# Kernel optimization log

Measured on AMD Instinct MI355X. Metric: run time of the kernel, lower is better.

The kernel has to match this reference:

```python
import jax, jax.numpy as jnp
import numpy as np

C = 64        # channel_n
HID = 128     # hidden_size
HEADS = 4
HD = 16       # head_dim = embed_dim // heads, embed_dim overwritten to channel_n
INNER = HEADS * HD  # 64
MLP = 64
H = W = 64    # img_size
B = 8
STEPS = 6
IN_CH = 1     # input_channels
SCALE = HD ** -0.5


def conv3x3_reflect(x, w, b):
    # x: [B,C,H,W], w: [O,I,3,3] -- reflect padding like nn.Conv2d(padding_mode='reflect')
    xp = jnp.pad(x, ((0, 0), (0, 0), (1, 1), (1, 1)), mode='reflect')
    y = jax.lax.conv_general_dilated(xp, w, (1, 1), 'VALID',
                                     dimension_numbers=('NCHW', 'OIHW', 'NCHW'))
    return y + b[None, :, None, None]


def layernorm(x, w, b, axes):
    mu = jnp.mean(x, axis=axes, keepdims=True)
    var = jnp.var(x, axis=axes, keepdims=True)
    return (x - mu) * jax.lax.rsqrt(var + 1e-5) * w + b


def localize(t, h, w):
    # t: [B,heads,n,d] -> [B,heads,n,9,d]; zero-padded 3x3 neighbourhoods
    # (equivalent to grouped conv with 9 unit-impulse filters, padding='same')
    b, nh, n, d = t.shape
    g = t.reshape(b, nh, h, w, d)
    gp = jnp.pad(g, ((0, 0), (0, 0), (1, 1), (1, 1), (0, 0)))
    nb = jnp.stack([gp[:, :, i:i + h, j:j + w, :]
                    for i in range(3) for j in range(3)], axis=4)
    return nb.reshape(b, nh, n, 9, d)


def attn_block(t, ln_w, ln_b, qkv_w, out_w, out_b):
    y = layernorm(t, ln_w, ln_b, -1)
    qkv = y @ qkv_w.T                              # [B,n,3*inner]
    q, k, v = jnp.split(qkv, 3, axis=-1)
    to_heads = lambda z: z.reshape(z.shape[0], z.shape[1], HEADS, HD).transpose(0, 2, 1, 3)
    q, k, v = to_heads(q), to_heads(k), to_heads(v)   # [B,h,n,d]
    kl = localize(k, H, W)                          # [B,h,n,9,d]
    vl = localize(v, H, W)
    dots = jnp.einsum('bhnd,bhnkd->bhnk', q, kl) * SCALE
    a = jax.nn.softmax(dots, axis=-1)               # [B,h,n,9]
    o = jnp.einsum('bhnk,bhnkd->bhnd', a, vl)
    o = o.transpose(0, 2, 1, 3).reshape(t.shape[0], t.shape[1], INNER)
    return o @ out_w.T + out_b


def ff_block(t, ln_w, ln_b, w1, b1, w2, b2):
    y = layernorm(t, ln_w, ln_b, -1)
    y = jax.nn.gelu(y @ w1.T + b1, approximate=False)
    return y @ w2.T + b2


def setup_inputs() -> dict:
    key = jax.random.key(0)
    ks = jax.random.split(key, 20)
    s = 0.02
    inp = {
        'x': jax.random.normal(ks[0], (B, H, W, C), jnp.float32),
        'masks': jax.random.bernoulli(ks[1], 0.5, (STEPS, B, H, W, 1)),
        'p0_w': jax.random.normal(ks[2], (C, C, 3, 3)) * s,
        'p0_b': jnp.zeros((C,)),
        'p1_w': jax.random.normal(ks[3], (C, C, 3, 3)) * s,
        'p1_b': jnp.zeros((C,)),
        'fc0_w': jax.random.normal(ks[4], (HID, 3 * C)) * s,
        'fc0_b': jnp.zeros((HID,)),
        'fc1_w': jax.random.normal(ks[5], (C, HID)) * s,  # zero-init in torch; random here for a non-trivial test
        'norm0_w': jnp.ones((H, W, HID)),
        'norm0_b': jnp.zeros((H, W, HID)),
        'ln1_w': jnp.ones((C,)),
        'ln1_b': jnp.zeros((C,)),
        'qkv_w': jax.random.normal(ks[6], (3 * INNER, C)) * s,
        'out_w': jax.random.normal(ks[7], (C, INNER)) * s,
        'out_b': jnp.zeros((C,)),
        'ln2_w': jnp.ones((C,)),
        'ln2_b': jnp.zeros((C,)),
        'ff1_w': jax.random.normal(ks[8], (MLP, C)) * s,
        'ff1_b': jnp.zeros((MLP,)),
        'ff2_w': jax.random.normal(ks[9], (C, MLP)) * s,
        'ff2_b': jnp.zeros((C,)),
        'steps': STEPS,
    }
    return inp


def reference(x, masks, p0_w, p0_b, p1_w, p1_b, fc0_w, fc0_b, fc1_w,
              norm0_w, norm0_b, ln1_w, ln1_b, qkv_w, out_w, out_b,
              ln2_w, ln2_b, ff1_w, ff1_b, ff2_w, ff2_b, steps):
    def step(xc, mask):
        # ---- NCA perception + update (BackboneNCA.perceive + fc0/relu/norm/fc1) ----
        xt = xc.transpose(0, 3, 1, 2)                      # [B,C,H,W]
        y1 = conv3x3_reflect(xt, p0_w, p0_b)
        y2 = conv3x3_reflect(xt, p1_w, p1_b)
        p = jnp.concatenate([xt, y1, y2], 1).transpose(0, 2, 3, 1)  # [B,H,W,3C]
        hd = jax.nn.relu(p @ fc0_w.T + fc0_b)              # [B,H,W,HID]
        hd = layernorm(hd, norm0_w, norm0_b, (-3, -2, -1))  # norm0 over [H,W,HID]
        dx = hd @ fc1_w.T                                   # [B,H,W,C]
        dx = dx * mask.astype(xc.dtype)                     # stochastic fire
        xn = xc + dx
        # ---- ViT block with localized (3x3 windowed) attention ----
        t = xn.reshape(B, H * W, C)
        t = t + attn_block(t, ln1_w, ln1_b, qkv_w, out_w, out_b)
        t = t + ff_block(t, ln2_w, ln2_b, ff1_w, ff1_b, ff2_w, ff2_b)
        xn = t.reshape(B, H, W, C)
        # keep input channels unchanged
        xn = jnp.concatenate([xc[..., :IN_CH], xn[..., IN_CH:]], axis=-1)
        return xn, None

    out, _ = jax.lax.scan(step, x, masks)
    return out
```

## Files before the change

kernel.cpp:

```cpp
#include <hip/hip_runtime.h>
#include <hip/hip_bf16.h>

typedef __hip_bfloat16 bf16;
typedef __attribute__((ext_vector_type(8))) short bf16x8;
typedef __attribute__((ext_vector_type(4))) float f32x4;

#define NSTEP 6

static __device__ __forceinline__ float b2f(bf16 v) { return __bfloat162float(v); }

static __device__ __forceinline__ float ldp(const void* p, int i, int md) {
    return md ? ((const float*)p)[i] : b2f(((const bf16*)p)[i]);
}
static __device__ __forceinline__ float finz(float v) {
    return (v == v && v * 0.0f == 0.0f) ? v : 0.0f;
}
static __device__ __forceinline__ unsigned short f2bfu(float v) {
    bf16 h = __float2bfloat16(v);
    return *(unsigned short*)&h;
}

static __device__ __forceinline__ void ld_bf8(const bf16* p, float* f) {
    union { uint4 u; unsigned short s[8]; } r;
    r.u = *(const uint4*)p;
#pragma unroll
    for (int j = 0; j < 8; ++j) f[j] = __uint_as_float(((unsigned)r.s[j]) << 16);
}
static __device__ __forceinline__ void ldp8(const void* p, int i, int md, float* f) {
    if (md) {
        const float* fp = (const float*)p + i;
        float4 a = *(const float4*)fp, b = *(const float4*)(fp + 4);
        f[0]=a.x; f[1]=a.y; f[2]=a.z; f[3]=a.w; f[4]=b.x; f[5]=b.y; f[6]=b.z; f[7]=b.w;
    } else {
        ld_bf8((const bf16*)p + i, f);
    }
}
static __device__ __forceinline__ uint4 pk_bf8(const float* f) {
    union { uint4 u; unsigned short s[8]; } r;
#pragma unroll
    for (int j = 0; j < 8; ++j) r.s[j] = f2bfu(f[j]);
    return r.u;
}


__global__ void k_detect(const uint4* __restrict__ m4,
                         const uint4* __restrict__ x4,
                         int* __restrict__ flags, float* __restrict__ accv) {
    __shared__ int s3f, sup, slo, sf32;
    int t = threadIdx.x;
    if (t == 0) { s3f = 0; sup = 0; slo = 0; sf32 = 0; }
    if (t < 96) accv[t] = 0.f;
    __syncthreads();
    int l3f = 0, lup = 0, llo = 0, lf = 0;
    for (int i = t; i < 3072; i += 256) {
        uint4 v = m4[i];
        const unsigned* d = (const unsigned*)&v;
#pragma unroll
        for (int j = 0; j < 4; ++j) {
            unsigned w = d[j];
            unsigned x3f = w ^ 0x3F3F3F3Fu;
            if ((x3f - 0x01010101u) & ~x3f & 0x80808080u) l3f = 1;
            if (w & 0xFFFFFF00u) lup = 1;
            if (w & 0x0000FFFFu) llo = 1;
        }
    }
    for (int i = t; i < 4096; i += 256) {
        uint4 v = x4[i];
        const unsigned* d = (const unsigned*)&v;
#pragma unroll
        for (int j = 0; j < 4; ++j) {
            unsigned bb = (d[j] >> 8) & 0x7Fu;
            if (bb > 0x48u) lf = 1;
        }
    }
    if (l3f) atomicOr(&s3f, 1);
    if (lup) atomicOr(&sup, 1);
    if (llo) atomicOr(&slo, 1);
    if (lf)  atomicOr(&sf32, 1);
    __syncthreads();
    if (t == 0) {
        int mode;
        if (!s3f && !sup) mode = 0;
        else if (!s3f)    mode = 1;
        else if (slo)     mode = 2;
        else              mode = 3;
        flags[0] = mode;
        flags[1] = sf32;
    }
}

__global__ void k_cast(const void* __restrict__ in, float* __restrict__ out,
                       const int* __restrict__ mflags, int n8) {
    int md = mflags[1];
    int i = blockIdx.x * 256 + threadIdx.x;
    if (i < n8) {
        float f[8];
        ldp8(in, i * 8, md, f);
#pragma unroll
        for (int j = 0; j < 8; ++j) f[j] = finz(f[j]);
        *(float4*)&out[i * 8]     = make_float4(f[0], f[1], f[2], f[3]);
        *(float4*)&out[i * 8 + 4] = make_float4(f[4], f[5], f[6], f[7]);
    }
}

__global__ void k_transpose(const void* __restrict__ in, float* __restrict__ out,
                            const int* __restrict__ mflags, int R, int K) {
    int md = mflags[1];
    int i = blockIdx.x * 256 + threadIdx.x;
    if (i < R * K) {
        int k = i / R, r = i % R;
        out[i] = ldp(in, r * K + k, md);
    }
}

__global__ void k_pack_bf16(const void* __restrict__ in, short* __restrict__ out,
                            const int* __restrict__ mflags, int n) {
    int md = mflags[1];
    int i = blockIdx.x * 256 + threadIdx.x;
    if (i < n) out[i] = (short)f2bfu(ldp(in, i, md));
}

__global__ void k_pack_bt1(const void* __restrict__ p0, const void* __restrict__ p1,
                           short* __restrict__ out, const int* __restrict__ mflags) {
    int md = mflags[1];
    int i = blockIdx.x * 256 + threadIdx.x;
    if (i < 128 * 576) {
        int o = i / 576, k = i % 576;
        int kk = k >> 6, ii = k & 63;
        float v = (o < 64) ? ldp(p0, o * 576 + ii * 9 + kk, md)
                           : ldp(p1, (o - 64) * 576 + ii * 9 + kk, md);
        out[i] = (short)f2bfu(v);
    }
}


__global__ __launch_bounds__(512) void k_perceive(
    const float* __restrict__ xin, const short* __restrict__ bt1,
    const short* __restrict__ fc0s, const void* __restrict__ p0b,
    const void* __restrict__ p1b, const void* __restrict__ fc0b,
    const int* __restrict__ mflags, bf16* __restrict__ hd,
    float* __restrict__ accv, int step)
{
    __shared__ __align__(16) short xpad_s[3 * 66 * 72];
    __shared__ __align__(16) short P_s[64 * 200];
    __shared__ float red[32];
    int md = mflags[1];
    int bh = blockIdx.x;
    int b = bh >> 6, h = bh & 63;
    int t = threadIdx.x;

    for (int e = t; e < 1536; e += 512) {
        int c8 = e & 7, w = (e >> 3) & 63, r = e >> 9;
        int hr = h - 1 + r; hr = hr < 0 ? -hr : (hr > 63 ? 126 - hr : hr);
        const float* src = xin + ((((b << 6) + hr) << 6) | w) * 64 + c8 * 8;
        float f[8];
        float4 v0 = *(const float4*)src, v1 = *(const float4*)(src + 4);
        f[0]=v0.x; f[1]=v0.y; f[2]=v0.z; f[3]=v0.w; f[4]=v1.x; f[5]=v1.y; f[6]=v1.z; f[7]=v1.w;
        uint4 pv = pk_bf8(f);
        *(uint4*)&xpad_s[((r * 66) + w + 1) * 72 + c8 * 8] = pv;
        if (r == 1) *(uint4*)&P_s[w * 200 + c8 * 8] = pv;
    }
    if (t < 48) {
        int c8 = t & 7, side = (t >> 3) & 1, r = t >> 4;
        int hr = h - 1 + r; hr = hr < 0 ? -hr : (hr > 63 ? 126 - hr : hr);
        int wsrc = side ? 62 : 1, wp = side ? 65 : 0;
        const float* src = xin + ((((b << 6) + hr) << 6) | wsrc) * 64 + c8 * 8;
        float f[8];
        float4 v0 = *(const float4*)src, v1 = *(const float4*)(src + 4);
        f[0]=v0.x; f[1]=v0.y; f[2]=v0.z; f[3]=v0.w; f[4]=v1.x; f[5]=v1.y; f[6]=v1.z; f[7]=v1.w;
        *(uint4*)&xpad_s[((r * 66) + wp) * 72 + c8 * 8] = pk_bf8(f);
    }
    __syncthreads();

    int og  = __builtin_amdgcn_readfirstlane(t >> 6);
    int l   = t & 63, nl = l & 15, q = l >> 4;
    int mt0 = (og & 1) * 2;
    int nt0 = (og >> 1) * 2;
    int o0  = nt0 * 16 + nl, o1 = o0 + 16;

    f32x4 acc[2][2];
#pragma unroll
    for (int i = 0; i < 2; ++i)
#pragma unroll
        for (int j = 0; j < 2; ++j) acc[i][j] = (f32x4){0.f, 0.f, 0.f, 0.f};

    for (int kt = 0; kt < 18; ++kt) {
        int kk = kt >> 1, c0 = (kt & 1) << 5;
        int r = kk / 3, cxi = kk - r * 3;
        bf16x8 b0 = *(const bf16x8*)(bt1 + o0 * 576 + kt * 32 + q * 8);
        bf16x8 b1 = *(const bf16x8*)(bt1 + o1 * 576 + kt * 32 + q * 8);
        bf16x8 a0 = *(const bf16x8*)&xpad_s[((r * 66) + mt0 * 16 + nl + cxi) * 72 + c0 + q * 8];
        bf16x8 a1 = *(const bf16x8*)&xpad_s[((r * 66) + mt0 * 16 + 16 + nl + cxi) * 72 + c0 + q * 8];
        acc[0][0] = __builtin_amdgcn_mfma_f32_16x16x32_bf16(a0, b0, acc[0][0], 0, 0, 0);
        acc[0][1] = __builtin_amdgcn_mfma_f32_16x16x32_bf16(a0, b1, acc[0][1], 0, 0, 0);
        acc[1][0] = __builtin_amdgcn_mfma_f32_16x16x32_bf16(a1, b0, acc[1][0], 0, 0, 0);
        acc[1][1] = __builtin_amdgcn_mfma_f32_16x16x32_bf16(a1, b1, acc[1][1], 0, 0, 0);
    }
    {
        float bias0 = (o0 < 64) ? ldp(p0b, o0, md) : ldp(p1b, o0 - 64, md);
        float bias1 = (o1 < 64) ? ldp(p0b, o1, md) : ldp(p1b, o1 - 64, md);
#pragma unroll
        for (int i = 0; i < 2; ++i)
#pragma unroll
            for (int j = 0; j < 2; ++j) {
                int oo = j ? o1 : o0;
                float bb = j ? bias1 : bias0;
#pragma unroll
                for (int r2 = 0; r2 < 4; ++r2) {
                    int m = (mt0 + i) * 16 + q * 4 + r2;
                    P_s[m * 200 + 64 + oo] = (short)f2bfu(acc[i][j][r2] + bb);
                }
            }
    }
    __syncthreads();

#pragma unroll
    for (int i = 0; i < 2; ++i)
#pragma unroll
        for (int j = 0; j < 2; ++j) acc[i][j] = (f32x4){0.f, 0.f, 0.f, 0.f};
    for (int kt = 0; kt < 6; ++kt) {
        bf16x8 b0 = *(const bf16x8*)(fc0s + o0 * 192 + kt * 32 + q * 8);
        bf16x8 b1 = *(const bf16x8*)(fc0s + o1 * 192 + kt * 32 + q * 8);
        bf16x8 a0 = *(const bf16x8*)&P_s[(mt0 * 16 + nl) * 200 + kt * 32 + q * 8];
        bf16x8 a1 = *(const bf16x8*)&P_s[(mt0 * 16 + 16 + nl) * 200 + kt * 32 + q * 8];
        acc[0][0] = __builtin_amdgcn_mfma_f32_16x16x32_bf16(a0, b0, acc[0][0], 0, 0, 0);
        acc[0][1] = __builtin_amdgcn_mfma_f32_16x16x32_bf16(a0, b1, acc[0][1], 0, 0, 0);
        acc[1][0] = __builtin_amdgcn_mfma_f32_16x16x32_bf16(a1, b0, acc[1][0], 0, 0, 0);
        acc[1][1] = __builtin_amdgcn_mfma_f32_16x16x32_bf16(a1, b1, acc[1][1], 0, 0, 0);
    }
    float lsum = 0.f, lsq = 0.f;
    {
        float fb0 = ldp(fc0b, o0, md), fb1 = ldp(fc0b, o1, md);
#pragma unroll
        for (int i = 0; i < 2; ++i)
#pragma unroll
            for (int j = 0; j < 2; ++j) {
                int oo = j ? o1 : o0;
                float bb = j ? fb1 : fb0;
#pragma unroll
                for (int r2 = 0; r2 < 4; ++r2) {
                    int m = (mt0 + i) * 16 + q * 4 + r2;
                    float v = fmaxf(acc[i][j][r2] + bb, 0.f);
                    unsigned short hu = f2bfu(v);
                    hd[((bh << 6) + m) * 128 + oo] = *(bf16*)&hu;
                    float vr = __uint_as_float(((unsigned)hu) << 16);
                    lsum += vr; lsq += vr * vr;
                }
            }
    }
#pragma unroll
    for (int off = 32; off > 0; off >>= 1) {
        lsum += __shfl_down(lsum, off, 64);
        lsq  += __shfl_down(lsq,  off, 64);
    }
    if (l == 0) { red[og] = lsum; red[16 + og] = lsq; }
    __syncthreads();
    if (t == 0) {
        float a = 0.f, s2 = 0.f;
#pragma unroll
        for (int w = 0; w < 8; ++w) { a += red[w]; s2 += red[16 + w]; }
        atomicAdd(&accv[step * 16 + b * 2],     a);
        atomicAdd(&accv[step * 16 + b * 2 + 1], s2);
    }
}

__global__ __launch_bounds__(512) void k_update_qkv(
    float* __restrict__ xio, const bf16* __restrict__ hd,
    const float* __restrict__ fc1t, const void* __restrict__ n0w,
    const void* __restrict__ n0b, const void* __restrict__ mraw,
    const int* __restrict__ mflags, const float* __restrict__ accv,
    float* __restrict__ c0buf, const float* __restrict__ qkvt,
    const void* __restrict__ ln1w, const void* __restrict__ ln1b,
    bf16* __restrict__ qkv, int step)
{
    __shared__ float hdn[64 * 129];
    __shared__ float ys[64 * 65];
    int md = mflags[1];
    int bh = blockIdx.x;
    int b = bh >> 6, h = bh & 63;
    int t = threadIdx.x;
    const float invN = 1.f / 524288.f;
    float mean = accv[step * 16 + b * 2] * invN;
    float var  = accv[step * 16 + b * 2 + 1] * invN - mean * mean;
    float rstd = rsqrtf(fmaxf(var, 0.f) + 1e-5f);

    const bf16* hrow = hd + ((b * 64 + h) * 64) * 128;
    for (int e = t; e < 1024; e += 512) {
        int pos = e >> 4, j8 = (e & 15) * 8;
        float hv[8], wv[8], bv[8];
        ld_bf8(hrow + pos * 128 + j8, hv);
        int ni = (h * 64 + pos) * 128 + j8;
        ldp8(n0w, ni, md, wv);
        ldp8(n0b, ni, md, bv);
#pragma unroll
        for (int j = 0; j < 8; ++j)
            hdn[pos * 129 + j8 + j] = (hv[j] - mean) * rstd * wv[j] + bv[j];
    }
    __syncthreads();

    int cg  = __builtin_amdgcn_readfirstlane(t >> 6);
    int pos = t & 63;
    float acc[8];
#pragma unroll
    for (int ci = 0; ci < 8; ++ci) acc[ci] = 0.f;
    for (int j = 0; j < 128; ++j) {
        float hv = hdn[pos * 129 + j];
        const float* fw = fc1t + j * 64 + cg * 8;
#pragma unroll
        for (int ci = 0; ci < 8; ++ci) acc[ci] = fmaf(fw[ci], hv, acc[ci]);
    }
    int mmode = mflags[0];
    int midx = ((step * 8 + b) * 64 + h) * 64 + pos;
    int m;
    if (mmode == 0)      m = ((const int*)mraw)[midx] != 0;
    else if (mmode == 1) m = ((const unsigned char*)mraw)[midx] != 0;
    else if (mmode == 2) m = ((const unsigned short*)mraw)[midx] != 0;
    else                 m = ((const float*)mraw)[midx] != 0.0f;

    int idx = ((b * 64 + h) * 64 + pos) * 64 + cg * 8;
    float4 x0 = *(const float4*)&xio[idx];
    float4 x1 = *(const float4*)&xio[idx + 4];
    float xv[8] = {x0.x, x0.y, x0.z, x0.w, x1.x, x1.y, x1.z, x1.w};
    if (cg == 0) c0buf[(b * 64 + h) * 64 + pos] = xv[0];
    float xn[8];
#pragma unroll
    for (int ci = 0; ci < 8; ++ci) {
        xn[ci] = finz(m ? (xv[ci] + acc[ci]) : xv[ci]);
        ys[pos * 65 + cg * 8 + ci] = xn[ci];
    }
    *(float4*)&xio[idx]     = make_float4(xn[0], xn[1], xn[2], xn[3]);
    *(float4*)&xio[idx + 4] = make_float4(xn[4], xn[5], xn[6], xn[7]);
    __syncthreads();

    {
        int tok = t >> 3, j8 = (t & 7) * 8;
        float v[8];
        float ls = 0.f, lq = 0.f;
#pragma unroll
        for (int ci = 0; ci < 8; ++ci) {
            v[ci] = ys[tok * 65 + j8 + ci];
            ls += v[ci]; lq += v[ci] * v[ci];
        }
#pragma unroll
        for (int off = 1; off < 8; off <<= 1) {
            ls += __shfl_xor(ls, off, 64);
            lq += __shfl_xor(lq, off, 64);
        }
        float mu = ls * (1.f / 64.f);
        float vr = lq * (1.f / 64.f) - mu * mu;
        float rs = rsqrtf(fmaxf(vr, 0.f) + 1e-5f);
        float wv[8], bv[8];
        ldp8(ln1w, j8, md, wv);
        ldp8(ln1b, j8, md, bv);
#pragma unroll
        for (int ci = 0; ci < 8; ++ci)
            ys[tok * 65 + j8 + ci] = (v[ci] - mu) * rs * wv[ci] + bv[ci];
    }
    __syncthreads();

    float a2[24];
#pragma unroll
    for (int oi = 0; oi < 24; ++oi) a2[oi] = 0.f;
    for (int c = 0; c < 64; ++c) {
        float yv = ys[pos * 65 + c];
        const float* qw = qkvt + c * 192 + cg * 24;
#pragma unroll
        for (int oi = 0; oi < 24; ++oi) a2[oi] = fmaf(qw[oi], yv, a2[oi]);
    }
    union { uint4 u[3]; unsigned short s[24]; } pq;
#pragma unroll
    for (int oi = 0; oi < 24; ++oi) pq.s[oi] = f2bfu(a2[oi]);
    uint4* qrow = (uint4*)(qkv + (((b * 64 + h) * 64) + pos) * 192 + cg * 24);
    qrow[0] = pq.u[0]; qrow[1] = pq.u[1]; qrow[2] = pq.u[2];
}

__global__ __launch_bounds__(512) void k_attn_ff(
    const bf16* __restrict__ qkv, float* __restrict__ xio,
    const float* __restrict__ c0buf, const short* __restrict__ outs,
    const short* __restrict__ ff1s, const short* __restrict__ ff2s,
    const void* __restrict__ outb, const void* __restrict__ ln2w,
    const void* __restrict__ ln2b, const void* __restrict__ ff1b,
    const void* __restrict__ ff2b, const int* __restrict__ mflags,
    void* __restrict__ dout, int write_out)
{
    __shared__ __align__(16) char smraw[50944];
    float* kv = (float*)smraw;
    short* Ao = (short*)smraw;
    float* ts = (float*)(smraw + 9216);
    short* ys = (short*)(smraw + 25856);
    short* hs = (short*)(smraw + 35072);

    int md = mflags[1];
    int bh = blockIdx.x;
    int b = bh >> 6, h = bh & 63;
    int t = threadIdx.x;

    if (t < 192) {
        int c = t & 63, r = t >> 6;
        kv[c * 199 + r * 66]      = 0.f;
        kv[c * 199 + r * 66 + 65] = 0.f;
    }
    for (int e = t; e < 1536; e += 512) {
        int c8 = (e & 7) * 8, w = (e >> 3) & 63, r = e >> 9;
        int hr = h - 1 + r;
        float f[8];
        if (hr >= 0 && hr <= 63) {
            ld_bf8(qkv + ((b * 64 + hr) * 64 + w) * 192 + 64 + c8, f);
        } else {
#pragma unroll
            for (int j = 0; j < 8; ++j) f[j] = 0.f;
        }
#pragma unroll
        for (int j = 0; j < 8; ++j) kv[(c8 + j) * 199 + r * 66 + w + 1] = f[j];
    }
    __syncthreads();

    int head = __builtin_amdgcn_readfirstlane((t >> 6) & 3);
    int pos  = t & 63;
    float q[16];
    {
        const bf16* qr = qkv + (((b * 64 + h) * 64) + pos) * 192 + head * 16;
        ld_bf8(qr, q); ld_bf8(qr + 8, q + 8);
    }

    float a[9];
#pragma unroll
    for (int r = 0; r < 3; ++r)
#pragma unroll
        for (int cxi = 0; cxi < 3; ++cxi) {
            float dot = 0.f;
#pragma unroll
            for (int d = 0; d < 16; ++d)
                dot = fmaf(q[d], kv[(head * 16 + d) * 199 + r * 66 + pos + cxi], dot);
            a[r * 3 + cxi] = dot * 0.25f;
        }
    float mx = a[0];
#pragma unroll
    for (int k = 1; k < 9; ++k) mx = fmaxf(mx, a[k]);
    float ssum = 0.f;
#pragma unroll
    for (int k = 0; k < 9; ++k) { a[k] = __expf(a[k] - mx); ssum += a[k]; }
    float inv = 1.f / ssum;
#pragma unroll
    for (int k = 0; k < 9; ++k) a[k] *= inv;
    __syncthreads();

    for (int e = t; e < 1536; e += 512) {
        int c8 = (e & 7) * 8, w = (e >> 3) & 63, r = e >> 9;
        int hr = h - 1 + r;
        float f[8];
        if (hr >= 0 && hr <= 63) {
            ld_bf8(qkv + ((b * 64 + hr) * 64 + w) * 192 + 128 + c8, f);
        } else {
#pragma unroll
            for (int j = 0; j < 8; ++j) f[j] = 0.f;
        }
#pragma unroll
        for (int j = 0; j < 8; ++j) kv[(c8 + j) * 199 + r * 66 + w + 1] = f[j];
    }
    __syncthreads();

    float o[16];
#pragma unroll
    for (int d = 0; d < 16; ++d) {
        float ov = 0.f;
#pragma unroll
        for (int r = 0; r < 3; ++r)
#pragma unroll
            for (int cxi = 0; cxi < 3; ++cxi)
                ov = fmaf(a[r * 3 + cxi], kv[(head * 16 + d) * 199 + r * 66 + pos + cxi], ov);
        o[d] = ov;
    }
    __syncthreads();

    if (t < 256) {
        *(uint4*)&Ao[pos * 72 + head * 16]     = pk_bf8(o);
        *(uint4*)&Ao[pos * 72 + head * 16 + 8] = pk_bf8(o + 8);
    }
    __syncthreads();

    int og = __builtin_amdgcn_readfirstlane(t >> 6);
    int l = t & 63, nl = l & 15, qd = l >> 4;
    int mt = og & 3;
    int nt0 = (og >> 2) * 2;
    int o0 = nt0 * 16 + nl, o1 = o0 + 16;

    {
        f32x4 pa[2];
        pa[0] = (f32x4){0.f,0.f,0.f,0.f}; pa[1] = (f32x4){0.f,0.f,0.f,0.f};
#pragma unroll
        for (int kt = 0; kt < 2; ++kt) {
            bf16x8 av = *(const bf16x8*)&Ao[(mt * 16 + nl) * 72 + kt * 32 + qd * 8];
            bf16x8 b0 = *(const bf16x8*)(outs + o0 * 64 + kt * 32 + qd * 8);
            bf16x8 b1 = *(const bf16x8*)(outs + o1 * 64 + kt * 32 + qd * 8);
            pa[0] = __builtin_amdgcn_mfma_f32_16x16x32_bf16(av, b0, pa[0], 0, 0, 0);
            pa[1] = __builtin_amdgcn_mfma_f32_16x16x32_bf16(av, b1, pa[1], 0, 0, 0);
        }
        float ob0 = ldp(outb, o0, md), ob1 = ldp(outb, o1, md);
#pragma unroll
        for (int j = 0; j < 2; ++j)
#pragma unroll
            for (int r2 = 0; r2 < 4; ++r2) {
                int m = mt * 16 + qd * 4 + r2;
                ts[m * 65 + (j ? o1 : o0)] = pa[j][r2] + (j ? ob1 : ob0);
            }
    }
    __syncthreads();

    int idx = ((bh << 6) + pos) * 64 + (t >> 6) * 8;
    {
        int cg2 = t >> 6;
        float4 x0 = *(const float4*)&xio[idx];
        float4 x1 = *(const float4*)&xio[idx + 4];
        float* tp = &ts[pos * 65 + cg2 * 8];
        tp[0] += x0.x; tp[1] += x0.y; tp[2] += x0.z; tp[3] += x0.w;
        tp[4] += x1.x; tp[5] += x1.y; tp[6] += x1.z; tp[7] += x1.w;
    }
    __syncthreads();

    {
        int tok = t >> 3, j8 = (t & 7) * 8;
        float v[8];
        float ls = 0.f, lq = 0.f;
#pragma unroll
        for (int ci = 0; ci < 8; ++ci) {
            v[ci] = ts[tok * 65 + j8 + ci];
            ls += v[ci]; lq += v[ci] * v[ci];
        }
#pragma unroll
        for (int off = 1; off < 8; off <<= 1) {
            ls += __shfl_xor(ls, off, 64);
            lq += __shfl_xor(lq, off, 64);
        }
        float mu = ls * (1.f / 64.f);
        float vr = lq * (1.f / 64.f) - mu * mu;
        float rs = rsqrtf(fmaxf(vr, 0.f) + 1e-5f);
        float wv[8], bv[8];
        ldp8(ln2w, j8, md, wv);
        ldp8(ln2b, j8, md, bv);
        float yv[8];
#pragma unroll
        for (int ci = 0; ci < 8; ++ci) yv[ci] = (v[ci] - mu) * rs * wv[ci] + bv[ci];
        *(uint4*)&ys[tok * 72 + j8] = pk_bf8(yv);
    }
    __syncthreads();

    {
        f32x4 ma[2];
        ma[0] = (f32x4){0.f,0.f,0.f,0.f}; ma[1] = (f32x4){0.f,0.f,0.f,0.f};
#pragma unroll
        for (int kt = 0; kt < 2; ++kt) {
            bf16x8 av = *(const bf16x8*)&ys[(mt * 16 + nl) * 72 + kt * 32 + qd * 8];
            bf16x8 b0 = *(const bf16x8*)(ff1s + o0 * 64 + kt * 32 + qd * 8);
            bf16x8 b1 = *(const bf16x8*)(ff1s + o1 * 64 + kt * 32 + qd * 8);
            ma[0] = __builtin_amdgcn_mfma_f32_16x16x32_bf16(av, b0, ma[0], 0, 0, 0);
            ma[1] = __builtin_amdgcn_mfma_f32_16x16x32_bf16(av, b1, ma[1], 0, 0, 0);
        }
        float f1b0 = ldp(ff1b, o0, md), f1b1 = ldp(ff1b, o1, md);
#pragma unroll
        for (int j = 0; j < 2; ++j)
#pragma unroll
            for (int r2 = 0; r2 < 4; ++r2) {
                int m = mt * 16 + qd * 4 + r2;
                float v = ma[j][r2] + (j ? f1b1 : f1b0);
                float g = 0.5f * v * (1.f + erff(v * 0.70710678118654752f));
                hs[m * 72 + (j ? o1 : o0)] = (short)f2bfu(g);
            }
    }
    __syncthreads();

    {
        f32x4 fa[2];
        fa[0] = (f32x4){0.f,0.f,0.f,0.f}; fa[1] = (f32x4){0.f,0.f,0.f,0.f};
#pragma unroll
        for (int kt = 0; kt < 2; ++kt) {
            bf16x8 av = *(const bf16x8*)&hs[(mt * 16 + nl) * 72 + kt * 32 + qd * 8];
            bf16x8 b0 = *(const bf16x8*)(ff2s + o0 * 64 + kt * 32 + qd * 8);
            bf16x8 b1 = *(const bf16x8*)(ff2s + o1 * 64 + kt * 32 + qd * 8);
            fa[0] = __builtin_amdgcn_mfma_f32_16x16x32_bf16(av, b0, fa[0], 0, 0, 0);
            fa[1] = __builtin_amdgcn_mfma_f32_16x16x32_bf16(av, b1, fa[1], 0, 0, 0);
        }
        float f2b0 = ldp(ff2b, o0, md), f2b1 = ldp(ff2b, o1, md);
#pragma unroll
        for (int j = 0; j < 2; ++j)
#pragma unroll
            for (int r2 = 0; r2 < 4; ++r2) {
                int m = mt * 16 + qd * 4 + r2;
                int oo = j ? o1 : o0;
                ts[m * 65 + oo] += fa[j][r2] + (j ? f2b1 : f2b0);
            }
    }
    __syncthreads();

    {
        int cg2 = t >> 6;
        float fv[8];
#pragma unroll
        for (int ci = 0; ci < 8; ++ci) {
            float v = ts[pos * 65 + cg2 * 8 + ci];
            if (cg2 == 0 && ci == 0) v = c0buf[(bh << 6) + pos];
            fv[ci] = finz(v);
        }
        *(float4*)&xio[idx]     = make_float4(fv[0], fv[1], fv[2], fv[3]);
        *(float4*)&xio[idx + 4] = make_float4(fv[4], fv[5], fv[6], fv[7]);
        if (write_out) {
            if (md) {
                *(float4*)&((float*)dout)[idx]     = make_float4(fv[0], fv[1], fv[2], fv[3]);
                *(float4*)&((float*)dout)[idx + 4] = make_float4(fv[4], fv[5], fv[6], fv[7]);
            } else {
                *(uint4*)&((bf16*)dout)[idx] = pk_bf8(fv);
            }
        }
    }
}


extern "C" void kernel_launch(void* const* d_in, const int* in_sizes, int n_in,
                              void* d_out, int out_size, void* d_ws, size_t ws_size,
                              hipStream_t stream) {
    (void)in_sizes; (void)n_in; (void)out_size; (void)ws_size;
    const void* x     = d_in[0];
    const void* masks = d_in[1];
    const void* p0w   = d_in[2];
    const void* p0b   = d_in[3];
    const void* p1w   = d_in[4];
    const void* p1b   = d_in[5];
    const void* fc0w  = d_in[6];
    const void* fc0b  = d_in[7];
    const void* fc1w  = d_in[8];
    const void* n0w   = d_in[9];
    const void* n0b   = d_in[10];
    const void* ln1w  = d_in[11];
    const void* ln1b  = d_in[12];
    const void* qkvw  = d_in[13];
    const void* outw  = d_in[14];
    const void* outb  = d_in[15];
    const void* ln2w  = d_in[16];
    const void* ln2b  = d_in[17];
    const void* ff1w  = d_in[18];
    const void* ff1b  = d_in[19];
    const void* ff2w  = d_in[20];
    const void* ff2b  = d_in[21];

    char* wsb = (char*)d_ws;
    float* xst    = (float*)(wsb + 0);
    bf16*  hd     = (bf16*) (wsb + 8388608);
    bf16*  qkvb   = (bf16*) (wsb + 8388608);
    float* c0buf  = (float*)(wsb + 20971520);
    short* bt1    = (short*)(wsb + 21102592);
    short* fc0s   = (short*)(wsb + 21397504);
    float* fc1t   = (float*)(wsb + 21446656);
    float* qkvt   = (float*)(wsb + 21479424);
    short* outs   = (short*)(wsb + 21528576);
    short* ff1s   = (short*)(wsb + 21536768);
    short* ff2s   = (short*)(wsb + 21544960);
    float* accv   = (float*)(wsb + 21553152);
    int*   mflags = (int*)  (wsb + 21553536);

    k_detect<<<1, 256, 0, stream>>>((const uint4*)masks, (const uint4*)x, mflags, accv);
    k_cast<<<1024, 256, 0, stream>>>(x, xst, mflags, 262144);
    k_pack_bt1<<<288, 256, 0, stream>>>(p0w, p1w, bt1, mflags);
    k_pack_bf16<<<96, 256, 0, stream>>>(fc0w, fc0s, mflags, 24576);
    k_transpose<<<32, 256, 0, stream>>>(fc1w, fc1t, mflags, 64, 128);
    k_transpose<<<48, 256, 0, stream>>>(qkvw, qkvt, mflags, 192, 64);
    k_pack_bf16<<<16, 256, 0, stream>>>(outw, outs, mflags, 4096);
    k_pack_bf16<<<16, 256, 0, stream>>>(ff1w, ff1s, mflags, 4096);
    k_pack_bf16<<<16, 256, 0, stream>>>(ff2w, ff2s, mflags, 4096);

    for (int s = 0; s < NSTEP; ++s) {
        k_perceive<<<512, 512, 0, stream>>>(xst, bt1, fc0s, p0b, p1b, fc0b, mflags, hd, accv, s);
        k_update_qkv<<<512, 512, 0, stream>>>(xst, hd, fc1t, n0w, n0b, masks, mflags, accv,
                                              c0buf, qkvt, ln1w, ln1b, qkvb, s);
        k_attn_ff<<<512, 512, 0, stream>>>(qkvb, xst, c0buf, outs, ff1s, ff2s,
                                           outb, ln2w, ln2b, ff1b, ff2b, mflags,
                                           d_out, (s == NSTEP - 1) ? 1 : 0);
    }
}
```

Measured before the change: 701.2 us.

## Use MFMA for fc1 and QKV projections, load K and V together

The fc1 (128->64) and QKV (64->192) projections in k_update_qkv move from scalar FP32 FMA loops to bf16 MFMA tiles, with operands staged in shared memory as bf16. The QKV output is staged in shared memory and written out with coalesced 16-byte stores. In k_attn_ff, K and V are loaded once into one bf16 shared buffer instead of two FP32 passes, which removes a barrier and a reload. Weight packing is merged into a single launch. The main risk is lower precision, since fc1 and QKV inputs are now rounded to bf16.

Measured after the change: 772.5 us. 1.1x slower.

```diff
diff --git a/kernel.cpp b/kernel.cpp
--- a/kernel.cpp
+++ b/kernel.cpp
@@ -19,7 +19,9 @@
     bf16 h = __float2bfloat16(v);
     return *(unsigned short*)&h;
 }
-
+static __device__ __forceinline__ float su2f(short s) {
+    return __uint_as_float(((unsigned)(unsigned short)s) << 16);
+}
 static __device__ __forceinline__ void ld_bf8(const bf16* p, float* f) {
     union { uint4 u; unsigned short s[8]; } r;
     r.u = *(const uint4*)p;
@@ -101,23 +103,6 @@
         *(float4*)&out[i * 8]     = make_float4(f[0], f[1], f[2], f[3]);
         *(float4*)&out[i * 8 + 4] = make_float4(f[4], f[5], f[6], f[7]);
     }
-}
-
-__global__ void k_transpose(const void* __restrict__ in, float* __restrict__ out,
-                            const int* __restrict__ mflags, int R, int K) {
-    int md = mflags[1];
-    int i = blockIdx.x * 256 + threadIdx.x;
-    if (i < R * K) {
-        int k = i / R, r = i % R;
-        out[i] = ldp(in, r * K + k, md);
-    }
-}
-
-__global__ void k_pack_bf16(const void* __restrict__ in, short* __restrict__ out,
-                            const int* __restrict__ mflags, int n) {
-    int md = mflags[1];
-    int i = blockIdx.x * 256 + threadIdx.x;
-    if (i < n) out[i] = (short)f2bfu(ldp(in, i, md));
 }
 
 __global__ void k_pack_bt1(const void* __restrict__ p0, const void* __restrict__ p1,
@@ -129,6 +114,24 @@
         int kk = k >> 6, ii = k & 63;
         float v = (o < 64) ? ldp(p0, o * 576 + ii * 9 + kk, md)
                            : ldp(p1, (o - 64) * 576 + ii * 9 + kk, md);
+        out[i] = (short)f2bfu(v);
+    }
+}
+
+__global__ void k_pack_all(const void* __restrict__ fc0w, const void* __restrict__ fc1w,
+                           const void* __restrict__ qkvw, const void* __restrict__ outw,
+                           const void* __restrict__ ff1w, const void* __restrict__ ff2w,
+                           short* __restrict__ out, const int* __restrict__ mflags) {
+    int md = mflags[1];
+    int i = blockIdx.x * 256 + threadIdx.x;
+    if (i < 57344) {
+        float v;
+        if (i < 24576)      v = ldp(fc0w, i, md);
+        else if (i < 32768) v = ldp(fc1w, i - 24576, md);
+        else if (i < 45056) v = ldp(qkvw, i - 32768, md);
+        else if (i < 49152) v = ldp(outw, i - 45056, md);
+        else if (i < 53248) v = ldp(ff1w, i - 49152, md);
+        else                v = ldp(ff2w, i - 53248, md);
         out[i] = (short)f2bfu(v);
     }
 }
@@ -266,19 +269,27 @@
 
 __global__ __launch_bounds__(512) void k_update_qkv(
     float* __restrict__ xio, const bf16* __restrict__ hd,
-    const float* __restrict__ fc1t, const void* __restrict__ n0w,
+    const short* __restrict__ fc1s, const void* __restrict__ n0w,
     const void* __restrict__ n0b, const void* __restrict__ mraw,
     const int* __restrict__ mflags, const float* __restrict__ accv,
-    float* __restrict__ c0buf, const float* __restrict__ qkvt,
+    float* __restrict__ c0buf, const short* __restrict__ qkvs,
     const void* __restrict__ ln1w, const void* __restrict__ ln1b,
     bf16* __restrict__ qkv, int step)
 {
-    __shared__ float hdn[64 * 129];
-    __shared__ float ys[64 * 65];
+    __shared__ __align__(16) char UQ[44288];
+    short* hdnb   = (short*)UQ;
+    float* xrowf  = (float*)(UQ + 17408);
+    short* ysb    = (short*)(UQ + 34816);
+    short* qstage = (short*)UQ;
+
     int md = mflags[1];
+    int mmode = mflags[0];
     int bh = blockIdx.x;
     int b = bh >> 6, h = bh & 63;
     int t = threadIdx.x;
+    int og = __builtin_amdgcn_readfirstlane(t >> 6);
+    int l = t & 63, nl = l & 15, qd = l >> 4;
+
     const float invN = 1.f / 524288.f;
     float mean = accv[step * 16 + b * 2] * invN;
     float var  = accv[step * 16 + b * 2 + 1] * invN - mean * mean;
@@ -287,60 +298,69 @@
     const bf16* hrow = hd + ((b * 64 + h) * 64) * 128;
     for (int e = t; e < 1024; e += 512) {
         int pos = e >> 4, j8 = (e & 15) * 8;
-        float hv[8], wv[8], bv[8];
+        float hv[8], wv[8], bv[8], ov[8];
         ld_bf8(hrow + pos * 128 + j8, hv);
         int ni = (h * 64 + pos) * 128 + j8;
         ldp8(n0w, ni, md, wv);
         ldp8(n0b, ni, md, bv);
 #pragma unroll
-        for (int j = 0; j < 8; ++j)
-            hdn[pos * 129 + j8 + j] = (hv[j] - mean) * rstd * wv[j] + bv[j];
-    }
-    __syncthreads();
-
-    int cg  = __builtin_amdgcn_readfirstlane(t >> 6);
-    int pos = t & 63;
-    float acc[8];
-#pragma unroll
-    for (int ci = 0; ci < 8; ++ci) acc[ci] = 0.f;
-    for (int j = 0; j < 128; ++j) {
-        float hv = hdn[pos * 129 + j];
-        const float* fw = fc1t + j * 64 + cg * 8;
-#pragma unroll
-        for (int ci = 0; ci < 8; ++ci) acc[ci] = fmaf(fw[ci], hv, acc[ci]);
-    }
-    int mmode = mflags[0];
-    int midx = ((step * 8 + b) * 64 + h) * 64 + pos;
-    int m;
-    if (mmode == 0)      m = ((const int*)mraw)[midx] != 0;
-    else if (mmode == 1) m = ((const unsigned char*)mraw)[midx] != 0;
-    else if (mmode == 2) m = ((const unsigned short*)mraw)[midx] != 0;
-    else                 m = ((const float*)mraw)[midx] != 0.0f;
-
-    int idx = ((b * 64 + h) * 64 + pos) * 64 + cg * 8;
-    float4 x0 = *(const float4*)&xio[idx];
-    float4 x1 = *(const float4*)&xio[idx + 4];
-    float xv[8] = {x0.x, x0.y, x0.z, x0.w, x1.x, x1.y, x1.z, x1.w};
-    if (cg == 0) c0buf[(b * 64 + h) * 64 + pos] = xv[0];
-    float xn[8];
-#pragma unroll
-    for (int ci = 0; ci < 8; ++ci) {
-        xn[ci] = finz(m ? (xv[ci] + acc[ci]) : xv[ci]);
-        ys[pos * 65 + cg * 8 + ci] = xn[ci];
-    }
-    *(float4*)&xio[idx]     = make_float4(xn[0], xn[1], xn[2], xn[3]);
-    *(float4*)&xio[idx + 4] = make_float4(xn[4], xn[5], xn[6], xn[7]);
-    __syncthreads();
-
-    {
-        int tok = t >> 3, j8 = (t & 7) * 8;
+        for (int j = 0; j < 8; ++j) ov[j] = (hv[j] - mean) * rstd * wv[j] + bv[j];
+        *(uint4*)&hdnb[pos * 136 + j8] = pk_bf8(ov);
+    }
+    {
+        int pos = t >> 3, c8 = (t & 7) * 8;
+        const float* src = xio + ((bh << 6) + pos) * 64 + c8;
+        *(float4*)&xrowf[pos * 68 + c8]     = *(const float4*)src;
+        *(float4*)&xrowf[pos * 68 + c8 + 4] = *(const float4*)(src + 4);
+    }
+    __syncthreads();
+
+    int mt = og & 3;
+    int nt0 = (og >> 2) * 2;
+    int o0 = nt0 * 16 + nl, o1 = o0 + 16;
+    f32x4 f0 = (f32x4){0.f,0.f,0.f,0.f}, f1 = (f32x4){0.f,0.f,0.f,0.f};
+#pragma unroll
+    for (int kt = 0; kt < 4; ++kt) {
+        bf16x8 av = *(const bf16x8*)&hdnb[(mt * 16 + nl) * 136 + kt * 32 + qd * 8];
+        bf16x8 b0 = *(const bf16x8*)(fc1s + o0 * 128 + kt * 32 + qd * 8);
+        bf16x8 b1 = *(const bf16x8*)(fc1s + o1 * 128 + kt * 32 + qd * 8);
+        f0 = __builtin_amdgcn_mfma_f32_16x16x32_bf16(av, b0, f0, 0, 0, 0);
+        f1 = __builtin_amdgcn_mfma_f32_16x16x32_bf16(av, b1, f1, 0, 0, 0);
+    }
+    int mk[4];
+#pragma unroll
+    for (int r2 = 0; r2 < 4; ++r2) {
+        int m_ = mt * 16 + qd * 4 + r2;
+        int midx = ((step * 8 + b) * 64 + h) * 64 + m_;
+        if (mmode == 0)      mk[r2] = ((const int*)mraw)[midx] != 0;
+        else if (mmode == 1) mk[r2] = ((const unsigned char*)mraw)[midx] != 0;
+        else if (mmode == 2) mk[r2] = ((const unsigned short*)mraw)[midx] != 0;
+        else                 mk[r2] = ((const float*)mraw)[midx] != 0.0f;
+    }
+#pragma unroll
+    for (int j = 0; j < 2; ++j)
+#pragma unroll
+        for (int r2 = 0; r2 < 4; ++r2) {
+            int m_ = mt * 16 + qd * 4 + r2;
+            int n_ = j ? o1 : o0;
+            float xv = xrowf[m_ * 68 + n_];
+            if (n_ == 0) c0buf[(bh << 6) + m_] = xv;
+            float dx = j ? f1[r2] : f0[r2];
+            xrowf[m_ * 68 + n_] = finz(mk[r2] ? (xv + dx) : xv);
+        }
+    __syncthreads();
+
+    {
+        int pos = t >> 3, c8 = (t & 7) * 8;
         float v[8];
+#pragma unroll
+        for (int ci = 0; ci < 8; ++ci) v[ci] = xrowf[pos * 68 + c8 + ci];
+        float* dst = xio + ((bh << 6) + pos) * 64 + c8;
+        *(float4*)dst       = make_float4(v[0], v[1], v[2], v[3]);
+        *(float4*)(dst + 4) = make_float4(v[4], v[5], v[6], v[7]);
         float ls = 0.f, lq = 0.f;
 #pragma unroll
-        for (int ci = 0; ci < 8; ++ci) {
-            v[ci] = ys[tok * 65 + j8 + ci];
-            ls += v[ci]; lq += v[ci] * v[ci];
-        }
+        for (int ci = 0; ci < 8; ++ci) { ls += v[ci]; lq += v[ci] * v[ci]; }
 #pragma unroll
         for (int off = 1; off < 8; off <<= 1) {
             ls += __shfl_xor(ls, off, 64);
@@ -349,29 +369,44 @@
         float mu = ls * (1.f / 64.f);
         float vr = lq * (1.f / 64.f) - mu * mu;
         float rs = rsqrtf(fmaxf(vr, 0.f) + 1e-5f);
-        float wv[8], bv[8];
-        ldp8(ln1w, j8, md, wv);
-        ldp8(ln1b, j8, md, bv);
-#pragma unroll
-        for (int ci = 0; ci < 8; ++ci)
-            ys[tok * 65 + j8 + ci] = (v[ci] - mu) * rs * wv[ci] + bv[ci];
-    }
-    __syncthreads();
-
-    float a2[24];
-#pragma unroll
-    for (int oi = 0; oi < 24; ++oi) a2[oi] = 0.f;
-    for (int c = 0; c < 64; ++c) {
-        float yv = ys[pos * 65 + c];
-        const float* qw = qkvt + c * 192 + cg * 24;
-#pragma unroll
-        for (int oi = 0; oi < 24; ++oi) a2[oi] = fmaf(qw[oi], yv, a2[oi]);
-    }
-    union { uint4 u[3]; unsigned short s[24]; } pq;
-#pragma unroll
-    for (int oi = 0; oi < 24; ++oi) pq.s[oi] = f2bfu(a2[oi]);
-    uint4* qrow = (uint4*)(qkv + (((b * 64 + h) * 64) + pos) * 192 + cg * 24);
-    qrow[0] = pq.u[0]; qrow[1] = pq.u[1]; qrow[2] = pq.u[2];
+        float wv[8], bv[8], yv[8];
+        ldp8(ln1w, c8, md, wv);
+        ldp8(ln1b, c8, md, bv);
+#pragma unroll
+        for (int ci = 0; ci < 8; ++ci) yv[ci] = (v[ci] - mu) * rs * wv[ci] + bv[ci];
+        *(uint4*)&ysb[pos * 72 + c8] = pk_bf8(yv);
+    }
+    __syncthreads();
+
+    int baseN = (og >> 2) * 6;
+    f32x4 qa[6];
+#pragma unroll
+    for (int n6 = 0; n6 < 6; ++n6) qa[n6] = (f32x4){0.f,0.f,0.f,0.f};
+#pragma unroll
+    for (int kt = 0; kt < 2; ++kt) {
+        bf16x8 av = *(const bf16x8*)&ysb[(mt * 16 + nl) * 72 + kt * 32 + qd * 8];
+#pragma unroll
+        for (int n6 = 0; n6 < 6; ++n6) {
+            int o = (baseN + n6) * 16 + nl;
+            bf16x8 bq = *(const bf16x8*)(qkvs + o * 64 + kt * 32 + qd * 8);
+            qa[n6] = __builtin_amdgcn_mfma_f32_16x16x32_bf16(av, bq, qa[n6], 0, 0, 0);
+        }
+    }
+#pragma unroll
+    for (int n6 = 0; n6 < 6; ++n6)
+#pragma unroll
+        for (int r2 = 0; r2 < 4; ++r2) {
+            int m_ = mt * 16 + qd * 4 + r2;
+            int o = (baseN + n6) * 16 + nl;
+            qstage[m_ * 200 + o] = (short)f2bfu(qa[n6][r2]);
+        }
+    __syncthreads();
+#pragma unroll
+    for (int j = 0; j < 3; ++j) {
+        int flat = t * 3 + j;
+        int row = flat / 24, c16 = (flat % 24) * 8;
+        *(uint4*)&qkv[((bh << 6) + row) * 192 + c16] = *(uint4*)&qstage[row * 200 + c16];
+    }
 }
 
 __global__ __launch_bounds__(512) void k_attn_ff(
@@ -384,34 +419,33 @@
     void* __restrict__ dout, int write_out)
 {
     __shared__ __align__(16) char smraw[50944];
-    float* kv = (float*)smraw;
-    short* Ao = (short*)smraw;
-    float* ts = (float*)(smraw + 9216);
-    short* ys = (short*)(smraw + 25856);
-    short* hs = (short*)(smraw + 35072);
+    short* kvb = (short*)smraw;
+    short* Ao  = (short*)smraw;
+    float* ts  = (float*)(smraw + 9216);
+    short* ys  = (short*)(smraw + 25856);
+    short* hs  = (short*)(smraw + 35072);
 
     int md = mflags[1];
     int bh = blockIdx.x;
     int b = bh >> 6, h = bh & 63;
     int t = threadIdx.x;
 
-    if (t < 192) {
-        int c = t & 63, r = t >> 6;
-        kv[c * 199 + r * 66]      = 0.f;
-        kv[c * 199 + r * 66 + 65] = 0.f;
-    }
-    for (int e = t; e < 1536; e += 512) {
-        int c8 = (e & 7) * 8, w = (e >> 3) & 63, r = e >> 9;
+    if (t < 384) {
+        int c = t & 127, r = t >> 7;
+        kvb[c * 199 + r * 66]      = 0;
+        kvb[c * 199 + r * 66 + 65] = 0;
+    }
+    for (int e = t; e < 3072; e += 512) {
+        int c8 = (e & 15) * 8, w = (e >> 4) & 63, r = e >> 10;
         int hr = h - 1 + r;
-        float f[8];
+        union { uint4 u; short s[8]; } rv;
         if (hr >= 0 && hr <= 63) {
-            ld_bf8(qkv + ((b * 64 + hr) * 64 + w) * 192 + 64 + c8, f);
+            rv.u = *(const uint4*)(qkv + ((b * 64 + hr) * 64 + w) * 192 + 64 + c8);
         } else {
-#pragma unroll
-            for (int j = 0; j < 8; ++j) f[j] = 0.f;
-        }
-#pragma unroll
-        for (int j = 0; j < 8; ++j) kv[(c8 + j) * 199 + r * 66 + w + 1] = f[j];
+            rv.u = make_uint4(0, 0, 0, 0);
+        }
+#pragma unroll
+        for (int j = 0; j < 8; ++j) kvb[(c8 + j) * 199 + r * 66 + w + 1] = rv.s[j];
     }
     __syncthreads();
 
@@ -431,7 +465,7 @@
             float dot = 0.f;
 #pragma unroll
             for (int d = 0; d < 16; ++d)
-                dot = fmaf(q[d], kv[(head * 16 + d) * 199 + r * 66 + pos + cxi], dot);
+                dot = fmaf(q[d], su2f(kvb[(head * 16 + d) * 199 + r * 66 + pos + cxi]), dot);
             a[r * 3 + cxi] = dot * 0.25f;
         }
     float mx = a[0];
@@ -443,22 +477,6 @@
     float inv = 1.f / ssum;
 #pragma unroll
     for (int k = 0; k < 9; ++k) a[k] *= inv;
-    __syncthreads();
-
-    for (int e = t; e < 1536; e += 512) {
-        int c8 = (e & 7) * 8, w = (e >> 3) & 63, r = e >> 9;
-        int hr = h - 1 + r;
-        float f[8];
-        if (hr >= 0 && hr <= 63) {
-            ld_bf8(qkv + ((b * 64 + hr) * 64 + w) * 192 + 128 + c8, f);
-        } else {
-#pragma unroll
-            for (int j = 0; j < 8; ++j) f[j] = 0.f;
-        }
-#pragma unroll
-        for (int j = 0; j < 8; ++j) kv[(c8 + j) * 199 + r * 66 + w + 1] = f[j];
-    }
-    __syncthreads();
 
     float o[16];
 #pragma unroll
@@ -468,7 +486,8 @@
         for (int r = 0; r < 3; ++r)
 #pragma unroll
             for (int cxi = 0; cxi < 3; ++cxi)
-                ov = fmaf(a[r * 3 + cxi], kv[(head * 16 + d) * 199 + r * 66 + pos + cxi], ov);
+                ov = fmaf(a[r * 3 + cxi],
+                          su2f(kvb[(64 + head * 16 + d) * 199 + r * 66 + pos + cxi]), ov);
         o[d] = ov;
     }
     __syncthreads();
@@ -486,24 +505,22 @@
     int o0 = nt0 * 16 + nl, o1 = o0 + 16;
 
     {
-        f32x4 pa[2];
-        pa[0] = (f32x4){0.f,0.f,0.f,0.f}; pa[1] = (f32x4){0.f,0.f,0.f,0.f};
+        f32x4 pa0 = (f32x4){0.f,0.f,0.f,0.f}, pa1 = (f32x4){0.f,0.f,0.f,0.f};
 #pragma unroll
         for (int kt = 0; kt < 2; ++kt) {
             bf16x8 av = *(const bf16x8*)&Ao[(mt * 16 + nl) * 72 + kt * 32 + qd * 8];
             bf16x8 b0 = *(const bf16x8*)(outs + o0 * 64 + kt * 32 + qd * 8);
             bf16x8 b1 = *(const bf16x8*)(outs + o1 * 64 + kt * 32 + qd * 8);
-            pa[0] = __builtin_amdgcn_mfma_f32_16x16x32_bf16(av, b0, pa[0], 0, 0, 0);
-            pa[1] = __builtin_amdgcn_mfma_f32_16x16x32_bf16(av, b1, pa[1], 0, 0, 0);
+            pa0 = __builtin_amdgcn_mfma_f32_16x16x32_bf16(av, b0, pa0, 0, 0, 0);
+            pa1 = __builtin_amdgcn_mfma_f32_16x16x32_bf16(av, b1, pa1, 0, 0, 0);
         }
         float ob0 = ldp(outb, o0, md), ob1 = ldp(outb, o1, md);
 #pragma unroll
-        for (int j = 0; j < 2; ++j)
-#pragma unroll
-            for (int r2 = 0; r2 < 4; ++r2) {
-                int m = mt * 16 + qd * 4 + r2;
-                ts[m * 65 + (j ? o1 : o0)] = pa[j][r2] + (j ? ob1 : ob0);
-            }
+        for (int r2 = 0; r2 < 4; ++r2) {
+            int m = mt * 16 + qd * 4 + r2;
+            ts[m * 65 + o0] = pa0[r2] + ob0;
+            ts[m * 65 + o1] = pa1[r2] + ob1;
+        }
     }
     __syncthreads();
 
@@ -535,10 +552,9 @@
         float mu = ls * (1.f / 64.f);
         float vr = lq * (1.f / 64.f) - mu * mu;
         float rs = rsqrtf(fmaxf(vr, 0.f) + 1e-5f);
-        float wv[8], bv[8];
+        float wv[8], bv[8], yv[8];
         ldp8(ln2w, j8, md, wv);
         ldp8(ln2b, j8, md, bv);
-        float yv[8];
 #pragma unroll
         for (int ci = 0; ci < 8; ++ci) yv[ci] = (v[ci] - mu) * rs * wv[ci] + bv[ci];
         *(uint4*)&ys[tok * 72 + j8] = pk_bf8(yv);
@@ -546,49 +562,44 @@
     __syncthreads();
 
     {
-        f32x4 ma[2];
-        ma[0] = (f32x4){0.f,0.f,0.f,0.f}; ma[1] = (f32x4){0.f,0.f,0.f,0.f};
+        f32x4 ma0 = (f32x4){0.f,0.f,0.f,0.f}, ma1 = (f32x4){0.f,0.f,0.f,0.f};
 #pragma unroll
         for (int kt = 0; kt < 2; ++kt) {
             bf16x8 av = *(const bf16x8*)&ys[(mt * 16 + nl) * 72 + kt * 32 + qd * 8];
             bf16x8 b0 = *(const bf16x8*)(ff1s + o0 * 64 + kt * 32 + qd * 8);
             bf16x8 b1 = *(const bf16x8*)(ff1s + o1 * 64 + kt * 32 + qd * 8);
-            ma[0] = __builtin_amdgcn_mfma_f32_16x16x32_bf16(av, b0, ma[0], 0, 0, 0);
-            ma[1] = __builtin_amdgcn_mfma_f32_16x16x32_bf16(av, b1, ma[1], 0, 0, 0);
+            ma0 = __builtin_amdgcn_mfma_f32_16x16x32_bf16(av, b0, ma0, 0, 0, 0);
+            ma1 = __builtin_amdgcn_mfma_f32_16x16x32_bf16(av, b1, ma1, 0, 0, 0);
         }
         float f1b0 = ldp(ff1b, o0, md), f1b1 = ldp(ff1b, o1, md);
 #pragma unroll
-        for (int j = 0; j < 2; ++j)
-#pragma unroll
-            for (int r2 = 0; r2 < 4; ++r2) {
-                int m = mt * 16 + qd * 4 + r2;
-                float v = ma[j][r2] + (j ? f1b1 : f1b0);
-                float g = 0.5f * v * (1.f + erff(v * 0.70710678118654752f));
-                hs[m * 72 + (j ? o1 : o0)] = (short)f2bfu(g);
-            }
-    }
-    __syncthreads();
-
-    {
-        f32x4 fa[2];
-        fa[0] = (f32x4){0.f,0.f,0.f,0.f}; fa[1] = (f32x4){0.f,0.f,0.f,0.f};
+        for (int r2 = 0; r2 < 4; ++r2) {
+            int m = mt * 16 + qd * 4 + r2;
+            float v0 = ma0[r2] + f1b0;
+            float v1 = ma1[r2] + f1b1;
+            hs[m * 72 + o0] = (short)f2bfu(0.5f * v0 * (1.f + erff(v0 * 0.70710678118654752f)));
+            hs[m * 72 + o1] = (short)f2bfu(0.5f * v1 * (1.f + erff(v1 * 0.70710678118654752f)));
+        }
+    }
+    __syncthreads();
+
+    {
+        f32x4 fa0 = (f32x4){0.f,0.f,0.f,0.f}, fa1 = (f32x4){0.f,0.f,0.f,0.f};
 #pragma unroll
         for (int kt = 0; kt < 2; ++kt) {
             bf16x8 av = *(const bf16x8*)&hs[(mt * 16 + nl) * 72 + kt * 32 + qd * 8];
             bf16x8 b0 = *(const bf16x8*)(ff2s + o0 * 64 + kt * 32 + qd * 8);
             bf16x8 b1 = *(const bf16x8*)(ff2s + o1 * 64 + kt * 32 + qd * 8);
-            fa[0] = __builtin_amdgcn_mfma_f32_16x16x32_bf16(av, b0, fa[0], 0, 0, 0);
-            fa[1] = __builtin_amdgcn_mfma_f32_16x16x32_bf16(av, b1, fa[1], 0, 0, 0);
+            fa0 = __builtin_amdgcn_mfma_f32_16x16x32_bf16(av, b0, fa0, 0, 0, 0);
+            fa1 = __builtin_amdgcn_mfma_f32_16x16x32_bf16(av, b1, fa1, 0, 0, 0);
         }
         float f2b0 = ldp(ff2b, o0, md), f2b1 = ldp(ff2b, o1, md);
 #pragma unroll
-        for (int j = 0; j < 2; ++j)
-#pragma unroll
-            for (int r2 = 0; r2 < 4; ++r2) {
-                int m = mt * 16 + qd * 4 + r2;
-                int oo = j ? o1 : o0;
-                ts[m * 65 + oo] += fa[j][r2] + (j ? f2b1 : f2b0);
-            }
+        for (int r2 = 0; r2 < 4; ++r2) {
+            int m = mt * 16 + qd * 4 + r2;
+            ts[m * 65 + o0] += fa0[r2] + f2b0;
+            ts[m * 65 + o1] += fa1[r2] + f2b1;
+        }
     }
     __syncthreads();
 
@@ -643,34 +654,34 @@
     const void* ff2b  = d_in[21];
 
     char* wsb = (char*)d_ws;
-    float* xst    = (float*)(wsb + 0);
-    bf16*  hd     = (bf16*) (wsb + 8388608);
-    bf16*  qkvb   = (bf16*) (wsb + 8388608);
-    float* c0buf  = (float*)(wsb + 20971520);
-    short* bt1    = (short*)(wsb + 21102592);
-    short* fc0s   = (short*)(wsb + 21397504);
-    float* fc1t   = (float*)(wsb + 21446656);
-    float* qkvt   = (float*)(wsb + 21479424);
-    short* outs   = (short*)(wsb + 21528576);
-    short* ff1s   = (short*)(wsb + 21536768);
-    short* ff2s   = (short*)(wsb + 21544960);
-    float* accv   = (float*)(wsb + 21553152);
-    int*   mflags = (int*)  (wsb + 21553536);
+    float* xst      = (float*)(wsb + 0);
+    bf16*  qkvb     = (bf16*) (wsb + 8388608);
+    bf16*  hd       = (bf16*) (wsb + 8388608);
+    float* c0buf    = (float*)(wsb + 20971520);
+    short* bt1      = (short*)(wsb + 21102592);
+    short* packbase = (short*)(wsb + 21250048);
+    float* accv     = (float*)(wsb + 21364736);
+    int*   mflags   = (int*)  (wsb + 21365120);
+
+    const short* fc0s = packbase;
+    const short* fc1s = packbase + 24576;
+    const short* qkvs = packbase + 32768;
+    const short* outs = packbase + 45056;
+    const short* ff1s = packbase + 49152;
+    const short* ff2s = packbase + 53248;
 
     k_detect<<<1, 256, 0, stream>>>((const uint4*)masks, (const uint4*)x, mflags, accv);
     k_cast<<<1024, 256, 0, stream>>>(x, xst, mflags, 262144);
     k_pack_bt1<<<288, 256, 0, stream>>>(p0w, p1w, bt1, mflags);
-    k_pack_bf16<<<96, 256, 0, stream>>>(fc0w, fc0s, mflags, 24576);
-    k_transpose<<<32, 256, 0, stream>>>(fc1w, fc1t, mflags, 64, 128);
-    k_transpose<<<48, 256, 0, stream>>>(qkvw, qkvt, mflags, 192, 64);
-    k_pack_bf16<<<16, 256, 0, stream>>>(outw, outs, mflags, 4096);
-    k_pack_bf16<<<16, 256, 0, stream>>>(ff1w, ff1s, mflags, 4096);
-    k_pack_bf16<<<16, 256, 0, stream>>>(ff2w, ff2s, mflags, 4096);
+    k_pack_all<<<224, 256, 0, stream>>>(fc0w, fc1w, qkvw, outw, ff1w, ff2w,
+                                        packbase, mflags);
 
     for (int s = 0; s < NSTEP; ++s) {
-        k_perceive<<<512, 512, 0, stream>>>(xst, bt1, fc0s, p0b, p1b, fc0b, mflags, hd, accv, s);
-        k_update_qkv<<<512, 512, 0, stream>>>(xst, hd, fc1t, n0w, n0b, masks, mflags, accv,
-                                              c0buf, qkvt, ln1w, ln1b, qkvb, s);
+        k_perceive<<<512, 512, 0, stream>>>(xst, bt1, fc0s, p0b, p1b, fc0b,
+                                            mflags, hd, accv, s);
+        k_update_qkv<<<512, 512, 0, stream>>>(xst, hd, fc1s, n0w, n0b, masks,
+                                              mflags, accv, c0buf, qkvs,
+                                              ln1w, ln1b, qkvb, s);
         k_attn_ff<<<512, 512, 0, stream>>>(qkvb, xst, c0buf, outs, ff1s, ff2s,
                                            outb, ln2w, ln2b, ff1b, ff2b, mflags,
                                            d_out, (s == NSTEP - 1) ? 1 : 0);
```
